# Kernel optimization log

Hardware: AMD Instinct MI355X
Metric: run time of the kernel (lower is better)

The kernel has to match this reference:

```python
import jax, jax.numpy as jnp
import numpy as np

N, DEG, D_FEAT, D_OUT = 50000, 32, 128, 256

def setup_inputs() -> dict:
    key = jax.random.key(0)
    k1, k2, k3 = jax.random.split(key, 3)
    features = jax.random.normal(k1, (N, D_FEAT), dtype=jnp.float32)
    edge_look_up = jax.random.randint(k2, (N, DEG), 0, N, dtype=jnp.int64)
    # glorot-uniform kernel, shape (2*D_FEAT, D_OUT)
    limit = np.sqrt(6.0 / (2 * D_FEAT + D_OUT)).astype(np.float32)
    kernel = jax.random.uniform(k3, (2 * D_FEAT, D_OUT), dtype=jnp.float32,
                                minval=-limit, maxval=limit)
    return {"features": features, "edge_look_up": edge_look_up, "kernel": kernel}

def reference(features, edge_look_up, kernel):
    # [1] neighborhood aggregation: gather neighbor features and mean-reduce
    neigh = features[edge_look_up]          # [N, DEG, D_FEAT] (irregular gather)
    agg = jnp.mean(neigh, axis=1)           # [N, D_FEAT]
    # [2] concat self features with aggregated neighbor vectors
    out = jnp.concatenate([features, agg], axis=-1)  # [N, 2*D_FEAT]
    # [4] dense matmul + [5] relu activation
    return jax.nn.relu(out @ kernel)        # [N, D_OUT]
```

## Files before the change

### kernel.cpp

```cpp
#include <hip/hip_runtime.h>

#define NN  50000
#define DEG 32
#define DF  128
#define DO  256
#define FEAT4 (NN * DF / 4)

typedef __bf16 bf16x8 __attribute__((ext_vector_type(8)));
typedef float  f32x4  __attribute__((ext_vector_type(4)));
typedef float  f32x2  __attribute__((ext_vector_type(2)));
typedef unsigned short u16x8 __attribute__((ext_vector_type(8)));

#if defined(__has_builtin)
#if __has_builtin(__builtin_amdgcn_cvt_pk_f32_fp8) && __has_builtin(__builtin_amdgcn_cvt_pk_fp8_f32)
#define HW_FP8 1
#endif
#endif
#ifndef HW_FP8
#define HW_FP8 0
#endif

__device__ __forceinline__ unsigned short f2bf(float f) {
    unsigned u = __float_as_uint(f);
    u += 0x7FFF + ((u >> 16) & 1);
    return (unsigned short)(u >> 16);
}

#if !HW_FP8
__device__ __forceinline__ unsigned enc1_fp8(float f) {
    unsigned u = __float_as_uint(f);
    unsigned s = (u >> 31) << 7;
    float a = fabsf(f);
    if (!(a > 0.f)) return s;
    if (a >= 448.f) return s | 0x7E;
    u = __float_as_uint(a);
    int e = (int)((u >> 23) & 255) - 127;
    if (e < -6) {
        unsigned m = (unsigned)(a * 512.f + 0.5f);
        if (m >= 8) return s | 0x08;
        return s | m;
    }
    unsigned mant = (u >> 20) & 7;
    unsigned rnd  = ((u >> 19) & 1) & (((u & 0x7FFFF) != 0) | ((u >> 20) & 1));
    unsigned enc  = ((unsigned)(e + 7) << 3) | mant;
    return s | (enc + rnd);
}
__device__ __forceinline__ float dec1_fp8(unsigned b) {
    unsigned s = (b >> 7) & 1, e = (b >> 3) & 15, m = b & 7;
    float v = (e == 0) ? (float)m * 0.001953125f
                       : __uint_as_float(((e - 7 + 127) << 23) | (m << 20));
    return s ? -v : v;
}
#endif

__device__ __forceinline__ unsigned enc4_fp8(float4 v) {
#if HW_FP8
    int pk = 0;
    pk = __builtin_amdgcn_cvt_pk_fp8_f32(v.x, v.y, pk, false);
    pk = __builtin_amdgcn_cvt_pk_fp8_f32(v.z, v.w, pk, true);
    return (unsigned)pk;
#else
    return enc1_fp8(v.x) | (enc1_fp8(v.y) << 8) | (enc1_fp8(v.z) << 16) | (enc1_fp8(v.w) << 24);
#endif
}

__global__ __launch_bounds__(256) void convert_kernel(
    const float* __restrict__ feat, const float* __restrict__ W,
    unsigned* __restrict__ feat8, unsigned short* __restrict__ Wt)
{
    const int gid = blockIdx.x * 256 + threadIdx.x;
    if (gid < FEAT4) {
        const float4 v = ((const float4*)feat)[gid];
        feat8[gid] = enc4_fp8(v);
    } else {
        const int t = gid - FEAT4;
        if (t < DO * DO) {
            const int n = t >> 8, k = t & 255;
            Wt[n * DO + k] = f2bf(W[k * DO + n]);
        }
    }
}

#define BM  64
#define BN  256
#define LDT 72

__global__ __launch_bounds__(512) void fused_kernel(
    const float*          __restrict__ feat,
    const unsigned*       __restrict__ feat8,
    const int*            __restrict__ edges,
    const unsigned short* __restrict__ Wt,
    float*                __restrict__ out)
{
    __shared__ __align__(16) unsigned short Asw[BM * LDT];
    __shared__ __align__(16) unsigned short Bsw[BN * LDT];

    const int tid = threadIdx.x;
    const int m0  = blockIdx.x * BM;

    const int l = tid & 15;
    u16x8 aggr[2];
    #pragma unroll
    for (int pass = 0; pass < 2; ++pass) {
        int node = m0 + pass * 32 + (tid >> 4);
        if (node >= NN) node = NN - 1;
        const int* e = edges + node * DEG;
        float a[8] = {0.f, 0.f, 0.f, 0.f, 0.f, 0.f, 0.f, 0.f};
        #pragma unroll
        for (int d = 0; d < DEG; ++d) {
            const int idx = e[d];
            const uint2 pk = *(const uint2*)(feat8 + (size_t)idx * (DF / 4) + l * 2);
#if HW_FP8
            const f32x2 v0 = __builtin_amdgcn_cvt_pk_f32_fp8((int)pk.x, false);
            const f32x2 v1 = __builtin_amdgcn_cvt_pk_f32_fp8((int)pk.x, true);
            const f32x2 v2 = __builtin_amdgcn_cvt_pk_f32_fp8((int)pk.y, false);
            const f32x2 v3 = __builtin_amdgcn_cvt_pk_f32_fp8((int)pk.y, true);
            a[0] += v0[0]; a[1] += v0[1]; a[2] += v1[0]; a[3] += v1[1];
            a[4] += v2[0]; a[5] += v2[1]; a[6] += v3[0]; a[7] += v3[1];
#else
            #pragma unroll
            for (int j = 0; j < 4; ++j) a[j]     += dec1_fp8((pk.x >> (8 * j)) & 255);
            #pragma unroll
            for (int j = 0; j < 4; ++j) a[4 + j] += dec1_fp8((pk.y >> (8 * j)) & 255);
#endif
        }
        const float s = 1.0f / (float)DEG;
        #pragma unroll
        for (int j = 0; j < 8; ++j) aggr[pass][j] = f2bf(a[j] * s);
    }

    const int wave = tid >> 6, lane = tid & 63;
    const int quad = lane >> 4, lr = lane & 15;
    const int wm   = (wave & 1) * 32;
    const int wn   = (wave >> 1) * 64;

    f32x4 acc[2][4] = {};

    for (int kc = 0; kc < 4; ++kc) {
        __syncthreads();

        if (kc < 2) {
            const int r = tid >> 3;
            const int c = (tid & 7) * 8;
            int node = m0 + r;
            if (node >= NN) node = NN - 1;
            const float* src = feat + (size_t)node * DF + kc * 64 + c;
            const float4 v0 = *(const float4*)(src);
            const float4 v1 = *(const float4*)(src + 4);
            u16x8 o;
            o[0] = f2bf(v0.x); o[1] = f2bf(v0.y); o[2] = f2bf(v0.z); o[3] = f2bf(v0.w);
            o[4] = f2bf(v1.x); o[5] = f2bf(v1.y); o[6] = f2bf(v1.z); o[7] = f2bf(v1.w);
            *(u16x8*)(Asw + r * LDT + c) = o;
        } else {
            if ((l >> 3) == (kc - 2)) {
                const int c = (l & 7) * 8;
                #pragma unroll
                for (int pass = 0; pass < 2; ++pass) {
                    const int r = pass * 32 + (tid >> 4);
                    *(u16x8*)(Asw + r * LDT + c) = aggr[pass];
                }
            }
        }

        #pragma unroll
        for (int it = 0; it < 4; ++it) {
            const int sidx = it * 512 + tid;
            const int r = sidx >> 3;
            const int c = (sidx & 7) * 8;
            *(u16x8*)(Bsw + r * LDT + c) =
                *(const u16x8*)(Wt + (size_t)r * DO + kc * 64 + c);
        }

        __syncthreads();

        #pragma unroll
        for (int kk = 0; kk < 64; kk += 32) {
            bf16x8 af[2], bfr[4];
            #pragma unroll
            for (int i = 0; i < 2; ++i)
                af[i] = *(const bf16x8*)(Asw + (wm + i * 16 + lr) * LDT + kk + quad * 8);
            #pragma unroll
            for (int i = 0; i < 4; ++i)
                bfr[i] = *(const bf16x8*)(Bsw + (wn + i * 16 + lr) * LDT + kk + quad * 8);
            #pragma unroll
            for (int mi = 0; mi < 2; ++mi)
                #pragma unroll
                for (int ni = 0; ni < 4; ++ni)
                    acc[mi][ni] = __builtin_amdgcn_mfma_f32_16x16x32_bf16(
                        af[mi], bfr[ni], acc[mi][ni], 0, 0, 0);
        }
    }

    #pragma unroll
    for (int mi = 0; mi < 2; ++mi) {
        #pragma unroll
        for (int r = 0; r < 4; ++r) {
            const int row = m0 + wm + mi * 16 + quad * 4 + r;
            if (row < NN) {
                #pragma unroll
                for (int ni = 0; ni < 4; ++ni) {
                    out[(size_t)row * DO + wn + ni * 16 + lr] =
                        fmaxf(acc[mi][ni][r], 0.f);
                }
            }
        }
    }
}

extern "C" void kernel_launch(void* const* d_in, const int* in_sizes, int n_in,
                              void* d_out, int out_size, void* d_ws, size_t ws_size,
                              hipStream_t stream)
{
    const float* feat  = (const float*)d_in[0];
    const int*   edges = (const int*)d_in[1];
    const float* W     = (const float*)d_in[2];
    float*       out   = (float*)d_out;

    unsigned*       feat8 = (unsigned*)d_ws;
    unsigned short* Wt    = (unsigned short*)(feat8 + (size_t)NN * DF / 4);

    convert_kernel<<<(FEAT4 + DO * DO + 255) / 256, 256, 0, stream>>>(
        feat, W, feat8, Wt);

    fused_kernel<<<(NN + BM - 1) / BM, 512, 0, stream>>>(
        feat, feat8, edges, Wt, out);
}
```

Measured before the change: 128.5 us.

## Halve row tile and overlap neighbor gathers with self-feature MFMA

Block tile shrinks from 64 to 32 rows, so each thread handles one node. All 32 edge indices are loaded as int4 vectors and all 32 fp8 neighbor gathers are issued up front into registers. The decode and sum of those gathers is deferred until after the first k-chunk of MFMA work, so gather latency overlaps with the self-feature matmul. The cost is more register pressure from 32 live uint2 values, which may reduce occupancy. The W tile is also reloaded for every 32-row block, doubling B-tile traffic per row.

After: 154.6 us. +20.3%, slower.

```diff
diff --git a/kernel.cpp b/kernel.cpp
--- a/kernel.cpp
+++ b/kernel.cpp
@@ -81,9 +81,9 @@
     }
 }
 
-#define BM  64
+#define BM  32
 #define BN  256
-#define LDT 72
+#define LDT 68
 
 __global__ __launch_bounds__(512) void fused_kernel(
     const float*          __restrict__ feat,
@@ -97,69 +97,44 @@
 
     const int tid = threadIdx.x;
     const int m0  = blockIdx.x * BM;
-
-    const int l = tid & 15;
-    u16x8 aggr[2];
+    const int l   = tid & 15;
+    const int rn  = tid >> 4;
+
+    int gnode = m0 + rn;
+    if (gnode >= NN) gnode = NN - 1;
+
+    const int4* e4 = (const int4*)(edges + (size_t)gnode * DEG);
+    int4 eidx[8];
     #pragma unroll
-    for (int pass = 0; pass < 2; ++pass) {
-        int node = m0 + pass * 32 + (tid >> 4);
-        if (node >= NN) node = NN - 1;
-        const int* e = edges + node * DEG;
-        float a[8] = {0.f, 0.f, 0.f, 0.f, 0.f, 0.f, 0.f, 0.f};
-        #pragma unroll
-        for (int d = 0; d < DEG; ++d) {
-            const int idx = e[d];
-            const uint2 pk = *(const uint2*)(feat8 + (size_t)idx * (DF / 4) + l * 2);
-#if HW_FP8
-            const f32x2 v0 = __builtin_amdgcn_cvt_pk_f32_fp8((int)pk.x, false);
-            const f32x2 v1 = __builtin_amdgcn_cvt_pk_f32_fp8((int)pk.x, true);
-            const f32x2 v2 = __builtin_amdgcn_cvt_pk_f32_fp8((int)pk.y, false);
-            const f32x2 v3 = __builtin_amdgcn_cvt_pk_f32_fp8((int)pk.y, true);
-            a[0] += v0[0]; a[1] += v0[1]; a[2] += v1[0]; a[3] += v1[1];
-            a[4] += v2[0]; a[5] += v2[1]; a[6] += v3[0]; a[7] += v3[1];
-#else
-            #pragma unroll
-            for (int j = 0; j < 4; ++j) a[j]     += dec1_fp8((pk.x >> (8 * j)) & 255);
-            #pragma unroll
-            for (int j = 0; j < 4; ++j) a[4 + j] += dec1_fp8((pk.y >> (8 * j)) & 255);
-#endif
-        }
-        const float s = 1.0f / (float)DEG;
-        #pragma unroll
-        for (int j = 0; j < 8; ++j) aggr[pass][j] = f2bf(a[j] * s);
+    for (int j = 0; j < 8; ++j) eidx[j] = e4[j];
+    uint2 pk[DEG];
+    #pragma unroll
+    for (int j = 0; j < 8; ++j) {
+        pk[4 * j + 0] = *(const uint2*)(feat8 + (size_t)eidx[j].x * (DF / 4) + l * 2);
+        pk[4 * j + 1] = *(const uint2*)(feat8 + (size_t)eidx[j].y * (DF / 4) + l * 2);
+        pk[4 * j + 2] = *(const uint2*)(feat8 + (size_t)eidx[j].z * (DF / 4) + l * 2);
+        pk[4 * j + 3] = *(const uint2*)(feat8 + (size_t)eidx[j].w * (DF / 4) + l * 2);
     }
 
     const int wave = tid >> 6, lane = tid & 63;
     const int quad = lane >> 4, lr = lane & 15;
-    const int wm   = (wave & 1) * 32;
-    const int wn   = (wave >> 1) * 64;
-
-    f32x4 acc[2][4] = {};
+    const int wn   = wave * 32;
+
+    u16x8 aggr;
+    f32x4 acc[2][2] = {};
 
     for (int kc = 0; kc < 4; ++kc) {
-        __syncthreads();
+        if (kc) __syncthreads();
 
         if (kc < 2) {
-            const int r = tid >> 3;
-            const int c = (tid & 7) * 8;
-            int node = m0 + r;
-            if (node >= NN) node = NN - 1;
-            const float* src = feat + (size_t)node * DF + kc * 64 + c;
-            const float4 v0 = *(const float4*)(src);
-            const float4 v1 = *(const float4*)(src + 4);
-            u16x8 o;
-            o[0] = f2bf(v0.x); o[1] = f2bf(v0.y); o[2] = f2bf(v0.z); o[3] = f2bf(v0.w);
-            o[4] = f2bf(v1.x); o[5] = f2bf(v1.y); o[6] = f2bf(v1.z); o[7] = f2bf(v1.w);
-            *(u16x8*)(Asw + r * LDT + c) = o;
-        } else {
-            if ((l >> 3) == (kc - 2)) {
-                const int c = (l & 7) * 8;
-                #pragma unroll
-                for (int pass = 0; pass < 2; ++pass) {
-                    const int r = pass * 32 + (tid >> 4);
-                    *(u16x8*)(Asw + r * LDT + c) = aggr[pass];
-                }
-            }
+            const int c = (tid & 15) * 4;
+            const float4 v = *(const float4*)(feat + (size_t)gnode * DF + kc * 64 + c);
+            ushort4 o;
+            o.x = f2bf(v.x); o.y = f2bf(v.y); o.z = f2bf(v.z); o.w = f2bf(v.w);
+            *(ushort4*)(Asw + rn * LDT + c) = o;
+        } else if ((l >> 3) == (kc - 2)) {
+            const int c = (l & 7) * 8;
+            *(u16x8*)(Asw + rn * LDT + c) = aggr;
         }
 
         #pragma unroll
@@ -175,19 +150,42 @@
 
         #pragma unroll
         for (int kk = 0; kk < 64; kk += 32) {
-            bf16x8 af[2], bfr[4];
+            bf16x8 af[2], bfr[2];
             #pragma unroll
             for (int i = 0; i < 2; ++i)
-                af[i] = *(const bf16x8*)(Asw + (wm + i * 16 + lr) * LDT + kk + quad * 8);
-            #pragma unroll
-            for (int i = 0; i < 4; ++i)
+                af[i] = *(const bf16x8*)(Asw + (i * 16 + lr) * LDT + kk + quad * 8);
+            #pragma unroll
+            for (int i = 0; i < 2; ++i)
                 bfr[i] = *(const bf16x8*)(Bsw + (wn + i * 16 + lr) * LDT + kk + quad * 8);
             #pragma unroll
             for (int mi = 0; mi < 2; ++mi)
                 #pragma unroll
-                for (int ni = 0; ni < 4; ++ni)
+                for (int ni = 0; ni < 2; ++ni)
                     acc[mi][ni] = __builtin_amdgcn_mfma_f32_16x16x32_bf16(
                         af[mi], bfr[ni], acc[mi][ni], 0, 0, 0);
+        }
+
+        if (kc == 0) {
+            float a[8] = {0.f, 0.f, 0.f, 0.f, 0.f, 0.f, 0.f, 0.f};
+            #pragma unroll
+            for (int d = 0; d < DEG; ++d) {
+#if HW_FP8
+                const f32x2 v0 = __builtin_amdgcn_cvt_pk_f32_fp8((int)pk[d].x, false);
+                const f32x2 v1 = __builtin_amdgcn_cvt_pk_f32_fp8((int)pk[d].x, true);
+                const f32x2 v2 = __builtin_amdgcn_cvt_pk_f32_fp8((int)pk[d].y, false);
+                const f32x2 v3 = __builtin_amdgcn_cvt_pk_f32_fp8((int)pk[d].y, true);
+                a[0] += v0[0]; a[1] += v0[1]; a[2] += v1[0]; a[3] += v1[1];
+                a[4] += v2[0]; a[5] += v2[1]; a[6] += v3[0]; a[7] += v3[1];
+#else
+                #pragma unroll
+                for (int j = 0; j < 4; ++j) a[j]     += dec1_fp8((pk[d].x >> (8 * j)) & 255);
+                #pragma unroll
+                for (int j = 0; j < 4; ++j) a[4 + j] += dec1_fp8((pk[d].y >> (8 * j)) & 255);
+#endif
+            }
+            const float s = 1.0f / (float)DEG;
+            #pragma unroll
+            for (int j = 0; j < 8; ++j) aggr[j] = f2bf(a[j] * s);
         }
     }
 
@@ -195,10 +193,10 @@
     for (int mi = 0; mi < 2; ++mi) {
         #pragma unroll
         for (int r = 0; r < 4; ++r) {
-            const int row = m0 + wm + mi * 16 + quad * 4 + r;
+            const int row = m0 + mi * 16 + quad * 4 + r;
             if (row < NN) {
                 #pragma unroll
-                for (int ni = 0; ni < 4; ++ni) {
+                for (int ni = 0; ni < 2; ++ni) {
                     out[(size_t)row * DO + wn + ni * 16 + lr] =
                         fmaxf(acc[mi][ni][r], 0.f);
                 }
```

## Halve row tile, stage full A in LDS, read weights directly from global

Applied to the files above, without the earlier changes.

Shrinks the per-block row tile from 64 to 32 nodes, so each thread aggregates one node instead of two. The whole 32x256 bf16 A tile (self features plus aggregated neighbours) now goes into shared memory once, behind a single barrier. The per-k-chunk weight staging in LDS is dropped, and each wave loads its B fragments straight from the bf16 weight buffer in global/L2. The aim is a smaller LDS footprint, fewer barriers and higher occupancy (launch bounds now request 8 blocks) to hide gather latency, at the cost of more redundant weight reads through cache per block.

Measured after the change: 159.4 us. 1.24x slower.

```diff
diff --git a/kernel.cpp b/kernel.cpp
--- a/kernel.cpp
+++ b/kernel.cpp
@@ -81,30 +81,38 @@
     }
 }
 
-#define BM  64
-#define BN  256
-#define LDT 72
+#define BM  32
+#define LDA 264
 
-__global__ __launch_bounds__(512) void fused_kernel(
+__global__ __launch_bounds__(512, 8) void fused_kernel(
     const float*          __restrict__ feat,
     const unsigned*       __restrict__ feat8,
     const int*            __restrict__ edges,
     const unsigned short* __restrict__ Wt,
     float*                __restrict__ out)
 {
-    __shared__ __align__(16) unsigned short Asw[BM * LDT];
-    __shared__ __align__(16) unsigned short Bsw[BN * LDT];
+    __shared__ __align__(16) unsigned short Asw[BM * LDA];
 
     const int tid = threadIdx.x;
     const int m0  = blockIdx.x * BM;
+    const int rn  = tid >> 4;
+    const int l   = tid & 15;
 
-    const int l = tid & 15;
-    u16x8 aggr[2];
-    #pragma unroll
-    for (int pass = 0; pass < 2; ++pass) {
-        int node = m0 + pass * 32 + (tid >> 4);
-        if (node >= NN) node = NN - 1;
-        const int* e = edges + node * DEG;
+    int gnode = m0 + rn;
+    if (gnode >= NN) gnode = NN - 1;
+
+    {
+        const float* src = feat + (size_t)gnode * DF + l * 8;
+        const float4 v0 = *(const float4*)(src);
+        const float4 v1 = *(const float4*)(src + 4);
+        u16x8 o;
+        o[0] = f2bf(v0.x); o[1] = f2bf(v0.y); o[2] = f2bf(v0.z); o[3] = f2bf(v0.w);
+        o[4] = f2bf(v1.x); o[5] = f2bf(v1.y); o[6] = f2bf(v1.z); o[7] = f2bf(v1.w);
+        *(u16x8*)(Asw + rn * LDA + l * 8) = o;
+    }
+
+    {
+        const int* e = edges + (size_t)gnode * DEG;
         float a[8] = {0.f, 0.f, 0.f, 0.f, 0.f, 0.f, 0.f, 0.f};
         #pragma unroll
         for (int d = 0; d < DEG; ++d) {
@@ -125,83 +133,45 @@
 #endif
         }
         const float s = 1.0f / (float)DEG;
+        u16x8 aggr;
         #pragma unroll
-        for (int j = 0; j < 8; ++j) aggr[pass][j] = f2bf(a[j] * s);
+        for (int j = 0; j < 8; ++j) aggr[j] = f2bf(a[j] * s);
+        *(u16x8*)(Asw + rn * LDA + 128 + l * 8) = aggr;
     }
+
+    __syncthreads();
 
     const int wave = tid >> 6, lane = tid & 63;
     const int quad = lane >> 4, lr = lane & 15;
-    const int wm   = (wave & 1) * 32;
+    const int wm   = (wave & 1) * 16;
     const int wn   = (wave >> 1) * 64;
 
-    f32x4 acc[2][4] = {};
+    f32x4 acc[4] = {};
 
+    #pragma unroll
     for (int kc = 0; kc < 4; ++kc) {
-        __syncthreads();
-
-        if (kc < 2) {
-            const int r = tid >> 3;
-            const int c = (tid & 7) * 8;
-            int node = m0 + r;
-            if (node >= NN) node = NN - 1;
-            const float* src = feat + (size_t)node * DF + kc * 64 + c;
-            const float4 v0 = *(const float4*)(src);
-            const float4 v1 = *(const float4*)(src + 4);
-            u16x8 o;
-            o[0] = f2bf(v0.x); o[1] = f2bf(v0.y); o[2] = f2bf(v0.z); o[3] = f2bf(v0.w);
-            o[4] = f2bf(v1.x); o[5] = f2bf(v1.y); o[6] = f2bf(v1.z); o[7] = f2bf(v1.w);
-            *(u16x8*)(Asw + r * LDT + c) = o;
-        } else {
-            if ((l >> 3) == (kc - 2)) {
-                const int c = (l & 7) * 8;
-                #pragma unroll
-                for (int pass = 0; pass < 2; ++pass) {
-                    const int r = pass * 32 + (tid >> 4);
-                    *(u16x8*)(Asw + r * LDT + c) = aggr[pass];
-                }
-            }
-        }
-
-        #pragma unroll
-        for (int it = 0; it < 4; ++it) {
-            const int sidx = it * 512 + tid;
-            const int r = sidx >> 3;
-            const int c = (sidx & 7) * 8;
-            *(u16x8*)(Bsw + r * LDT + c) =
-                *(const u16x8*)(Wt + (size_t)r * DO + kc * 64 + c);
-        }
-
-        __syncthreads();
-
         #pragma unroll
         for (int kk = 0; kk < 64; kk += 32) {
-            bf16x8 af[2], bfr[4];
+            const int kb = kc * 64 + kk + quad * 8;
+            const bf16x8 af = *(const bf16x8*)(Asw + (wm + lr) * LDA + kb);
             #pragma unroll
-            for (int i = 0; i < 2; ++i)
-                af[i] = *(const bf16x8*)(Asw + (wm + i * 16 + lr) * LDT + kk + quad * 8);
-            #pragma unroll
-            for (int i = 0; i < 4; ++i)
-                bfr[i] = *(const bf16x8*)(Bsw + (wn + i * 16 + lr) * LDT + kk + quad * 8);
-            #pragma unroll
-            for (int mi = 0; mi < 2; ++mi)
-                #pragma unroll
-                for (int ni = 0; ni < 4; ++ni)
-                    acc[mi][ni] = __builtin_amdgcn_mfma_f32_16x16x32_bf16(
-                        af[mi], bfr[ni], acc[mi][ni], 0, 0, 0);
+            for (int ni = 0; ni < 4; ++ni) {
+                const bf16x8 bfr =
+                    *(const bf16x8*)(Wt + (size_t)(wn + ni * 16 + lr) * DO + kb);
+                acc[ni] = __builtin_amdgcn_mfma_f32_16x16x32_bf16(
+                    af, bfr, acc[ni], 0, 0, 0);
+            }
         }
     }
 
     #pragma unroll
-    for (int mi = 0; mi < 2; ++mi) {
-        #pragma unroll
-        for (int r = 0; r < 4; ++r) {
-            const int row = m0 + wm + mi * 16 + quad * 4 + r;
-            if (row < NN) {
-                #pragma unroll
-                for (int ni = 0; ni < 4; ++ni) {
-                    out[(size_t)row * DO + wn + ni * 16 + lr] =
-                        fmaxf(acc[mi][ni][r], 0.f);
-                }
+    for (int r = 0; r < 4; ++r) {
+        const int row = m0 + wm + quad * 4 + r;
+        if (row < NN) {
+            #pragma unroll
+            for (int ni = 0; ni < 4; ++ni) {
+                out[(size_t)row * DO + wn + ni * 16 + lr] =
+                    fmaxf(acc[ni][r], 0.f);
             }
         }
     }
```
